# Performance work log

Measured on AMD Instinct MI355X. Metric: run time of the kernel, lower is better.

## Reference

```python
import jax, jax.numpy as jnp
import numpy as np
from jax import lax

V, DM, DS, DC, EXP = 32000, 1024, 16, 4, 2
DI = EXP * DM            # 2048 inner dim
DTR = (DM + 15) // 16    # 64  dt_rank
B, L = 2, 2048


def setup_inputs() -> dict:
    key = jax.random.key(0)
    ks = jax.random.split(key, 10)
    tokens = jax.random.randint(ks[0], (B, L), 0, V)
    embed = jax.random.normal(ks[1], (V, DM), jnp.float32) * 0.02
    in_proj_w = jax.random.normal(ks[2], (2 * DI, DM), jnp.float32) * (DM ** -0.5)
    conv_w = jax.random.normal(ks[3], (DI, DC), jnp.float32) * 0.2
    conv_b = jnp.zeros((DI,), jnp.float32)
    x_proj_w = jax.random.normal(ks[4], (DTR + 2 * DS, DI), jnp.float32) * (DI ** -0.5)
    dt_proj_w = jax.random.normal(ks[5], (DI, DTR), jnp.float32) * (DTR ** -0.5)
    # mamba-style dt bias init: softplus^{-1}(uniform in [1e-3, ~0.1])
    dt = 1e-3 + jax.random.uniform(ks[6], (DI,), jnp.float32) * 0.1
    dt_proj_b = jnp.log(jnp.expm1(dt))
    # S4D-real init: A = -[1..d_state] per channel
    A_log = jnp.log(jnp.broadcast_to(jnp.arange(1, DS + 1, dtype=jnp.float32), (DI, DS)))
    D = jnp.ones((DI,), jnp.float32)
    out_proj_w = jax.random.normal(ks[7], (DM, DI), jnp.float32) * (DI ** -0.5)
    head_w = jax.random.normal(ks[8], (V, DM), jnp.float32) * 0.02
    head_b = jnp.zeros((V,), jnp.float32)
    return dict(tokens=tokens, embed=embed, in_proj_w=in_proj_w, conv_w=conv_w,
                conv_b=conv_b, x_proj_w=x_proj_w, dt_proj_w=dt_proj_w,
                dt_proj_b=dt_proj_b, A_log=A_log, D=D, out_proj_w=out_proj_w,
                head_w=head_w, head_b=head_b)


def mamba_block(emb, in_proj_w, conv_w, conv_b, x_proj_w, dt_proj_w, dt_proj_b,
                A_log, D, out_proj_w):
    # emb: (B, L, DM)
    xz = jnp.einsum('bld,ed->ble', emb, in_proj_w)      # (B, L, 2*DI)
    x, z = jnp.split(xz, 2, axis=-1)
    # depthwise causal conv1d over time, then SiLU
    xt = x.transpose(0, 2, 1)                            # (B, DI, L)
    xc = lax.conv_general_dilated(xt, conv_w[:, None, :], (1,), [(DC - 1, 0)],
                                  feature_group_count=DI)
    x = jax.nn.silu(xc + conv_b[:, None]).transpose(0, 2, 1)  # (B, L, DI)
    # input-dependent dt, B, C
    dbc = jnp.einsum('bld,ed->ble', x, x_proj_w)         # (B, L, DTR+2*DS)
    dt = dbc[..., :DTR]
    Bm = dbc[..., DTR:DTR + DS]                          # (B, L, DS)
    Cm = dbc[..., DTR + DS:]                             # (B, L, DS)
    dt = jax.nn.softplus(jnp.einsum('blr,dr->bld', dt, dt_proj_w) + dt_proj_b)
    A = -jnp.exp(A_log)                                  # (DI, DS)

    def step(h, inp):
        dt_t, B_t, C_t, u_t = inp                        # (B,DI),(B,DS),(B,DS),(B,DI)
        dA = jnp.exp(dt_t[:, :, None] * A)               # (B, DI, DS)
        h = dA * h + dt_t[:, :, None] * B_t[:, None, :] * u_t[:, :, None]
        y = jnp.einsum('bds,bs->bd', h, C_t)
        return h, y

    h0 = jnp.zeros((x.shape[0], DI, DS), x.dtype)
    _, ys = lax.scan(step, h0, (dt.transpose(1, 0, 2), Bm.transpose(1, 0, 2),
                                Cm.transpose(1, 0, 2), x.transpose(1, 0, 2)))
    y = ys.transpose(1, 0, 2) + x * D                    # skip connection D*u
    y = y * jax.nn.silu(z)                               # gate
    return jnp.einsum('bld,ed->ble', y, out_proj_w)      # (B, L, DM)


def reference(tokens, embed, in_proj_w, conv_w, conv_b, x_proj_w, dt_proj_w,
              dt_proj_b, A_log, D, out_proj_w, head_w, head_b):
    emb = embed[tokens]                                  # (B, L, DM)
    y = mamba_block(emb, in_proj_w, conv_w, conv_b, x_proj_w, dt_proj_w,
                    dt_proj_b, A_log, D, out_proj_w)
    return jnp.einsum('bld,vd->blv', y, head_w) + head_b  # (B, L, V) logits
```

## Files before the change

kernel.cpp:

```cpp
#include <hip/hip_runtime.h>

typedef unsigned short ushort_t;
typedef __bf16 bf16x8 __attribute__((ext_vector_type(8)));
typedef float f32x4 __attribute__((ext_vector_type(4)));

constexpr int V_  = 32000;
constexpr int DM_ = 1024;
constexpr int DS_ = 16;
constexpr int DI_ = 2048;
constexpr int DTR_= 64;
constexpr int B_  = 2;
constexpr int L_  = 2048;
constexpr int M_  = B_ * L_;
constexpr int NXZ_= 2 * DI_;

constexpr size_t OFF_W_IN   = 0;
constexpr size_t OFF_W_OUT  = OFF_W_IN   + (size_t)NXZ_*DM_*2;
constexpr size_t OFF_W_HEAD = OFF_W_OUT  + (size_t)DM_*DI_*2;
constexpr size_t OFF_EMB    = OFF_W_HEAD + (size_t)V_*DM_*2;
constexpr size_t OFF_XZ     = OFF_EMB    + (size_t)M_*DM_*2;
constexpr size_t OFF_X      = OFF_XZ     + (size_t)M_*NXZ_*4;
constexpr size_t OFF_DBC    = OFF_X      + (size_t)M_*DI_*4;
constexpr size_t OFF_DT     = OFF_DBC    + (size_t)M_*96*4;
constexpr size_t OFF_Y      = OFF_DT     + (size_t)M_*DI_*4;
constexpr size_t OFF_MO     = OFF_Y      + (size_t)M_*DI_*2;

__device__ __forceinline__ ushort_t f2bf(float f) {
  union { float f; unsigned u; } v; v.f = f;
  unsigned r = v.u + 0x7FFFu + ((v.u >> 16) & 1u);
  return (ushort_t)(r >> 16);
}

__device__ __forceinline__ void async16(const void* g, void* l) {
  __builtin_amdgcn_global_load_lds(
      (const __attribute__((address_space(1))) unsigned int*)g,
      (__attribute__((address_space(3))) unsigned int*)l, 16, 0, 0);
}

__global__ __launch_bounds__(256) void cvt_bf16_kernel(
    const float* __restrict__ in, ushort_t* __restrict__ out, int n4) {
  int i = blockIdx.x * 256 + threadIdx.x;
  if (i >= n4) return;
  float4 v = ((const float4*)in)[i];
  ushort4 o;
  o.x = f2bf(v.x); o.y = f2bf(v.y); o.z = f2bf(v.z); o.w = f2bf(v.w);
  ((ushort4*)out)[i] = o;
}

__global__ __launch_bounds__(256) void gather_kernel(
    const int* __restrict__ tokens, const float* __restrict__ embed,
    ushort_t* __restrict__ out) {
  int i = blockIdx.x * 256 + threadIdx.x;
  int row = i >> 8;
  int c4 = i & 255;
  int tok = tokens[row];
  float4 v = ((const float4*)(embed + (size_t)tok * DM_))[c4];
  ushort4 o;
  o.x = f2bf(v.x); o.y = f2bf(v.y); o.z = f2bf(v.z); o.w = f2bf(v.w);
  ((ushort4*)out)[(size_t)row * 256 + c4] = o;
}

template <int EPI>
__global__ __launch_bounds__(256) void gemm_bt_kernel(
    const ushort_t* __restrict__ A, const ushort_t* __restrict__ Bw,
    float* __restrict__ Cf, ushort_t* __restrict__ Cb,
    const float* __restrict__ bias, int Ncols, int K) {
  __shared__ __attribute__((aligned(16))) ushort_t lds_a[4 * 128 * 8];
  __shared__ __attribute__((aligned(16))) ushort_t lds_b[4 * 128 * 8];
  const int tid  = threadIdx.x;
  const int lane = tid & 63;
  const int wave = tid >> 6;
  const int wm = wave & 1;
  const int wn = wave >> 1;
  const int row0 = blockIdx.y * 128;
  const int col0 = blockIdx.x * 128;

  f32x4 acc[4][4];
#pragma unroll
  for (int i = 0; i < 4; ++i)
#pragma unroll
    for (int j = 0; j < 4; ++j) acc[i][j] = f32x4{0.f, 0.f, 0.f, 0.f};

  const int sA0 = 2 * wave, sA1 = 2 * wave + 1;
  const int iA0 = sA0 * 64 + lane, iA1 = sA1 * 64 + lane;
  const ushort_t* pa0 = A  + (size_t)(row0 + (iA0 & 127)) * K + (iA0 >> 7) * 8;
  const ushort_t* pa1 = A  + (size_t)(row0 + (iA1 & 127)) * K + (iA1 >> 7) * 8;
  const ushort_t* pb0 = Bw + (size_t)(col0 + (iA0 & 127)) * K + (iA0 >> 7) * 8;
  const ushort_t* pb1 = Bw + (size_t)(col0 + (iA1 & 127)) * K + (iA1 >> 7) * 8;
  ushort_t* la0 = lds_a + sA0 * 512;
  ushort_t* la1 = lds_a + sA1 * 512;
  ushort_t* lb0 = lds_b + sA0 * 512;
  ushort_t* lb1 = lds_b + sA1 * 512;

  const int q = lane >> 4;
  const int r = lane & 15;

  for (int k0 = 0; k0 < K; k0 += 32) {
    async16(pa0 + k0, la0);
    async16(pa1 + k0, la1);
    async16(pb0 + k0, lb0);
    async16(pb1 + k0, lb1);
    __syncthreads();
    bf16x8 af[4], bfr[4];
#pragma unroll
    for (int i = 0; i < 4; ++i) {
      af[i]  = *(const bf16x8*)(lds_a + ((size_t)q * 128 + wm * 64 + i * 16 + r) * 8);
      bfr[i] = *(const bf16x8*)(lds_b + ((size_t)q * 128 + wn * 64 + i * 16 + r) * 8);
    }
#pragma unroll
    for (int i = 0; i < 4; ++i)
#pragma unroll
      for (int j = 0; j < 4; ++j)
        acc[i][j] = __builtin_amdgcn_mfma_f32_16x16x32_bf16(af[i], bfr[j], acc[i][j], 0, 0, 0);
    __syncthreads();
  }

#pragma unroll
  for (int i = 0; i < 4; ++i) {
#pragma unroll
    for (int j = 0; j < 4; ++j) {
      const int col = col0 + wn * 64 + j * 16 + r;
#pragma unroll
      for (int t = 0; t < 4; ++t) {
        const int row = row0 + wm * 64 + i * 16 + q * 4 + t;
        const float v = acc[i][j][t];
        if (EPI == 0) {
          Cf[(size_t)row * Ncols + col] = v;
        } else if (EPI == 1) {
          Cb[(size_t)row * Ncols + col] = f2bf(v);
        } else {
          Cf[(size_t)row * Ncols + col] = v + bias[col];
        }
      }
    }
  }
}

__global__ __launch_bounds__(256) void conv_silu_kernel(
    const float* __restrict__ xz, const float* __restrict__ conv_w,
    const float* __restrict__ conv_b, float* __restrict__ x_f32) {
  int i = blockIdx.x * 256 + threadIdx.x;
  int d = i & (DI_ - 1);
  int l = (i >> 11) & (L_ - 1);
  int b = i >> 22;
  const float4 w = ((const float4*)conv_w)[d];
  size_t rb = ((size_t)(b * L_ + l)) * NXZ_ + d;
  float acc = conv_b[d] + w.w * xz[rb];
  if (l >= 1) acc += w.z * xz[rb - NXZ_];
  if (l >= 2) acc += w.y * xz[rb - 2 * (size_t)NXZ_];
  if (l >= 3) acc += w.x * xz[rb - 3 * (size_t)NXZ_];
  float s = acc / (1.f + __expf(-acc));
  x_f32[i] = s;
}

__global__ __launch_bounds__(256) void xproj_kernel(
    const float* __restrict__ x, const float* __restrict__ w,
    float* __restrict__ dbc) {
  __shared__ __attribute__((aligned(16))) float sx[DI_];
  int row = blockIdx.x;
  const float4* xr = (const float4*)(x + (size_t)row * DI_);
  for (int j = threadIdx.x; j < DI_ / 4; j += 256) ((float4*)sx)[j] = xr[j];
  __syncthreads();
  if (threadIdx.x < 96) {
    const float4* wr = (const float4*)(w + (size_t)threadIdx.x * DI_);
    float acc = 0.f;
    for (int k = 0; k < DI_ / 4; ++k) {
      float4 a = ((const float4*)sx)[k];
      float4 bb = wr[k];
      acc += a.x * bb.x + a.y * bb.y + a.z * bb.z + a.w * bb.w;
    }
    dbc[(size_t)row * 96 + threadIdx.x] = acc;
  }
}

__global__ __launch_bounds__(256) void dtproj_kernel(
    const float* __restrict__ dbc, const float* __restrict__ w,
    const float* __restrict__ bias, float* __restrict__ dt_full) {
  __shared__ __attribute__((aligned(16))) float sdt[DTR_];
  int row = blockIdx.x;
  if (threadIdx.x < 16)
    ((float4*)sdt)[threadIdx.x] = ((const float4*)(dbc + (size_t)row * 96))[threadIdx.x];
  __syncthreads();
#pragma unroll
  for (int jj = 0; jj < 8; ++jj) {
    int d = threadIdx.x + jj * 256;
    const float4* wr = (const float4*)(w + (size_t)d * DTR_);
    float acc = bias[d];
#pragma unroll
    for (int k = 0; k < DTR_ / 4; ++k) {
      float4 a = ((const float4*)sdt)[k];
      float4 bb = wr[k];
      acc += a.x * bb.x + a.y * bb.y + a.z * bb.z + a.w * bb.w;
    }
    float sp = (acc > 15.f) ? acc : log1pf(__expf(acc));
    dt_full[(size_t)row * DI_ + d] = sp;
  }
}

__global__ __launch_bounds__(256) void scan_kernel(
    const float* __restrict__ dt_full, const float* __restrict__ x_f32,
    const float* __restrict__ xz, const float* __restrict__ dbc,
    const float* __restrict__ A_log, const float* __restrict__ Dvec,
    ushort_t* __restrict__ y_bf) {
  const int b  = blockIdx.x >> 7;
  const int d0 = (blockIdx.x & 127) << 4;
  const int tid = threadIdx.x;
  const int ch = tid >> 4;
  const int s  = tid & 15;
  const int d  = d0 + ch;
  const float a  = -__expf(A_log[(size_t)d * DS_ + s]);
  const float Dd = Dvec[d];
  float h = 0.f;
  __shared__ float s_dt[64][16], s_u[64][16], s_z[64][16], s_B[64][16], s_C[64][16];
  const size_t rowbase = (size_t)b * L_;
  for (int l0 = 0; l0 < L_; l0 += 64) {
    __syncthreads();
    for (int i = tid; i < 1024; i += 256) {
      int ll = i >> 4, j = i & 15;
      size_t row = rowbase + l0 + ll;
      s_dt[ll][j] = dt_full[row * DI_ + d0 + j];
      s_u [ll][j] = x_f32 [row * DI_ + d0 + j];
      s_z [ll][j] = xz    [row * NXZ_ + DI_ + d0 + j];
      s_B [ll][j] = dbc   [row * 96 + DTR_ + j];
      s_C [ll][j] = dbc   [row * 96 + DTR_ + DS_ + j];
    }
    __syncthreads();
    for (int t = 0; t < 64; ++t) {
      float dt = s_dt[t][ch];
      float u  = s_u[t][ch];
      float dA = __expf(dt * a);
      h = dA * h + dt * u * s_B[t][s];
      float p = h * s_C[t][s];
      p += __shfl_xor(p, 8, 16);
      p += __shfl_xor(p, 4, 16);
      p += __shfl_xor(p, 2, 16);
      p += __shfl_xor(p, 1, 16);
      if (s == 0) {
        float y = p + u * Dd;
        float z = s_z[t][ch];
        y *= z / (1.f + __expf(-z));
        y_bf[(rowbase + l0 + t) * DI_ + d] = f2bf(y);
      }
    }
  }
}

extern "C" void kernel_launch(void* const* d_in, const int* in_sizes, int n_in,
                              void* d_out, int out_size, void* d_ws, size_t ws_size,
                              hipStream_t stream) {
  const int*   tokens     = (const int*)d_in[0];
  const float* embed      = (const float*)d_in[1];
  const float* in_proj_w  = (const float*)d_in[2];
  const float* conv_w     = (const float*)d_in[3];
  const float* conv_b     = (const float*)d_in[4];
  const float* x_proj_w   = (const float*)d_in[5];
  const float* dt_proj_w  = (const float*)d_in[6];
  const float* dt_proj_b  = (const float*)d_in[7];
  const float* A_log      = (const float*)d_in[8];
  const float* Dvec       = (const float*)d_in[9];
  const float* out_proj_w = (const float*)d_in[10];
  const float* head_w     = (const float*)d_in[11];
  const float* head_b     = (const float*)d_in[12];
  float* out = (float*)d_out;

  char* ws = (char*)d_ws;
  ushort_t* w_in_bf   = (ushort_t*)(ws + OFF_W_IN);
  ushort_t* w_out_bf  = (ushort_t*)(ws + OFF_W_OUT);
  ushort_t* w_head_bf = (ushort_t*)(ws + OFF_W_HEAD);
  ushort_t* emb_bf    = (ushort_t*)(ws + OFF_EMB);
  float*    xz        = (float*)   (ws + OFF_XZ);
  float*    x_f32     = (float*)   (ws + OFF_X);
  float*    dbc       = (float*)   (ws + OFF_DBC);
  float*    dt_full   = (float*)   (ws + OFF_DT);
  ushort_t* y_bf      = (ushort_t*)(ws + OFF_Y);
  ushort_t* mo_bf     = (ushort_t*)(ws + OFF_MO);

  cvt_bf16_kernel<<<(NXZ_ * DM_ / 4) / 256, 256, 0, stream>>>(in_proj_w, w_in_bf, NXZ_ * DM_ / 4);
  cvt_bf16_kernel<<<(DM_ * DI_ / 4) / 256, 256, 0, stream>>>(out_proj_w, w_out_bf, DM_ * DI_ / 4);
  cvt_bf16_kernel<<<(V_ * DM_ / 4) / 256, 256, 0, stream>>>(head_w, w_head_bf, V_ * DM_ / 4);
  gather_kernel<<<(M_ * DM_ / 4) / 256, 256, 0, stream>>>(tokens, embed, emb_bf);
  gemm_bt_kernel<0><<<dim3(NXZ_ / 128, M_ / 128), 256, 0, stream>>>(
      emb_bf, w_in_bf, xz, nullptr, nullptr, NXZ_, DM_);
  conv_silu_kernel<<<(M_ * DI_) / 256, 256, 0, stream>>>(xz, conv_w, conv_b, x_f32);
  xproj_kernel<<<M_, 256, 0, stream>>>(x_f32, x_proj_w, dbc);
  dtproj_kernel<<<M_, 256, 0, stream>>>(dbc, dt_proj_w, dt_proj_b, dt_full);
  scan_kernel<<<B_ * (DI_ / 16), 256, 0, stream>>>(dt_full, x_f32, xz, dbc, A_log, Dvec, y_bf);
  gemm_bt_kernel<1><<<dim3(DM_ / 128, M_ / 128), 256, 0, stream>>>(
      y_bf, w_out_bf, nullptr, mo_bf, nullptr, DM_, DI_);
  gemm_bt_kernel<2><<<dim3(V_ / 128, M_ / 128), 256, 0, stream>>>(
      mo_bf, w_head_bf, out, nullptr, head_b, V_, DM_);
}
```

Baseline: 2.600 ms.

## Double-buffer scan inputs and batch the recurrence into 16-step groups

The selective-scan kernel now prefetches the next 64-step chunk of dt, u, z, B and C into registers while the current chunk is computed, then stores them into a second shared-memory buffer. This hides global-load latency behind compute. The time loop is also restructured into groups of 16 steps: the exp and input terms are computed up front, the serial recurrence runs alone, and the shuffle reductions and gated outputs are batched. Doubling shared memory and holding extra register arrays may lower occupancy.

```diff
diff --git a/kernel.cpp b/kernel.cpp
--- a/kernel.cpp
+++ b/kernel.cpp
@@ -211,37 +211,91 @@
   const float a  = -__expf(A_log[(size_t)d * DS_ + s]);
   const float Dd = Dvec[d];
   float h = 0.f;
-  __shared__ float s_dt[64][16], s_u[64][16], s_z[64][16], s_B[64][16], s_C[64][16];
+  __shared__ float s_dt[2][64][16], s_u[2][64][16], s_z[2][64][16],
+                   s_B[2][64][16], s_C[2][64][16];
   const size_t rowbase = (size_t)b * L_;
-  for (int l0 = 0; l0 < L_; l0 += 64) {
+
+  int ll_[4], j_[4];
+#pragma unroll
+  for (int rr = 0; rr < 4; ++rr) {
+    int i = tid + rr * 256;
+    ll_[rr] = i >> 4;
+    j_[rr] = i & 15;
+  }
+
+#pragma unroll
+  for (int rr = 0; rr < 4; ++rr) {
+    const size_t row = rowbase + ll_[rr];
+    s_dt[0][ll_[rr]][j_[rr]] = dt_full[row * DI_ + d0 + j_[rr]];
+    s_u [0][ll_[rr]][j_[rr]] = x_f32 [row * DI_ + d0 + j_[rr]];
+    s_z [0][ll_[rr]][j_[rr]] = xz    [row * NXZ_ + DI_ + d0 + j_[rr]];
+    s_B [0][ll_[rr]][j_[rr]] = dbc   [row * 96 + DTR_ + j_[rr]];
+    s_C [0][ll_[rr]][j_[rr]] = dbc   [row * 96 + DTR_ + DS_ + j_[rr]];
+  }
+  __syncthreads();
+
+  for (int chunk = 0; chunk < L_ / 64; ++chunk) {
+    const int cur = chunk & 1;
+    const bool more = (chunk + 1 < L_ / 64);
+    float rdt[4], ru[4], rz[4], rB[4], rC[4];
+    if (more) {
+      const int l1 = (chunk + 1) * 64;
+#pragma unroll
+      for (int rr = 0; rr < 4; ++rr) {
+        const size_t row = rowbase + l1 + ll_[rr];
+        rdt[rr] = dt_full[row * DI_ + d0 + j_[rr]];
+        ru [rr] = x_f32 [row * DI_ + d0 + j_[rr]];
+        rz [rr] = xz    [row * NXZ_ + DI_ + d0 + j_[rr]];
+        rB [rr] = dbc   [row * 96 + DTR_ + j_[rr]];
+        rC [rr] = dbc   [row * 96 + DTR_ + DS_ + j_[rr]];
+      }
+    }
+#pragma unroll 1
+    for (int t0 = 0; t0 < 64; t0 += 16) {
+      float dA[16], dB[16], p[16];
+#pragma unroll
+      for (int t = 0; t < 16; ++t) {
+        const float dtv = s_dt[cur][t0 + t][ch];
+        const float uv  = s_u [cur][t0 + t][ch];
+        dA[t] = __expf(dtv * a);
+        dB[t] = dtv * uv * s_B[cur][t0 + t][s];
+      }
+#pragma unroll
+      for (int t = 0; t < 16; ++t) {
+        h = dA[t] * h + dB[t];
+        p[t] = h * s_C[cur][t0 + t][s];
+      }
+#pragma unroll
+      for (int t = 0; t < 16; ++t) p[t] += __shfl_xor(p[t], 8, 16);
+#pragma unroll
+      for (int t = 0; t < 16; ++t) p[t] += __shfl_xor(p[t], 4, 16);
+#pragma unroll
+      for (int t = 0; t < 16; ++t) p[t] += __shfl_xor(p[t], 2, 16);
+#pragma unroll
+      for (int t = 0; t < 16; ++t) p[t] += __shfl_xor(p[t], 1, 16);
+      if (s == 0) {
+#pragma unroll
+        for (int t = 0; t < 16; ++t) {
+          const float uv = s_u[cur][t0 + t][ch];
+          float y = p[t] + uv * Dd;
+          const float zv = s_z[cur][t0 + t][ch];
+          y *= zv / (1.f + __expf(-zv));
+          y_bf[(rowbase + chunk * 64 + t0 + t) * DI_ + d] = f2bf(y);
+        }
+      }
+    }
+    if (more) {
+      const int nb = cur ^ 1;
+#pragma unroll
+      for (int rr = 0; rr < 4; ++rr) {
+        s_dt[nb][ll_[rr]][j_[rr]] = rdt[rr];
+        s_u [nb][ll_[rr]][j_[rr]] = ru [rr];
+        s_z [nb][ll_[rr]][j_[rr]] = rz [rr];
+        s_B [nb][ll_[rr]][j_[rr]] = rB [rr];
+        s_C [nb][ll_[rr]][j_[rr]] = rC [rr];
+      }
+    }
     __syncthreads();
-    for (int i = tid; i < 1024; i += 256) {
-      int ll = i >> 4, j = i & 15;
-      size_t row = rowbase + l0 + ll;
-      s_dt[ll][j] = dt_full[row * DI_ + d0 + j];
-      s_u [ll][j] = x_f32 [row * DI_ + d0 + j];
-      s_z [ll][j] = xz    [row * NXZ_ + DI_ + d0 + j];
-      s_B [ll][j] = dbc   [row * 96 + DTR_ + j];
-      s_C [ll][j] = dbc   [row * 96 + DTR_ + DS_ + j];
-    }
-    __syncthreads();
-    for (int t = 0; t < 64; ++t) {
-      float dt = s_dt[t][ch];
-      float u  = s_u[t][ch];
-      float dA = __expf(dt * a);
-      h = dA * h + dt * u * s_B[t][s];
-      float p = h * s_C[t][s];
-      p += __shfl_xor(p, 8, 16);
-      p += __shfl_xor(p, 4, 16);
-      p += __shfl_xor(p, 2, 16);
-      p += __shfl_xor(p, 1, 16);
-      if (s == 0) {
-        float y = p + u * Dd;
-        float z = s_z[t][ch];
-        y *= z / (1.f + __expf(-z));
-        y_bf[(rowbase + l0 + t) * DI_ + d] = f2bf(y);
-      }
-    }
   }
 }
 
```

Measured after the change: 2.287 ms. -12.0%, faster.
